# Kernel optimization log

Hardware: AMD Instinct MI355X
Metric: run time of the kernel (lower is better)

Reference implementation:

```python
import jax, jax.numpy as jnp
import numpy as np

V, D, M, C, L = 100000, 256, 4096, 4096, 32
PAD = 0
EPS = 1e-8  # torch CosineSimilarity default eps


def setup_inputs() -> dict:
    key = jax.random.key(0)
    ks = jax.random.split(key, 6)
    xs = jax.random.randint(ks[0], (1, L), 0, V)
    mems = jax.random.randint(ks[1], (M, L), 0, V)
    ys = jax.random.randint(ks[2], (1, L), 0, V)
    cands = jax.random.randint(ks[3], (C, L), 0, V)
    lt = jax.random.normal(ks[4], (V, D), dtype=jnp.float32) * 0.02
    lt = lt.at[PAD].set(0.0)  # nn.Embedding padding_idx row is zero
    freqs = jax.random.uniform(ks[5], (V,), dtype=jnp.float32, minval=0.05, maxval=1.0)
    return {"xs": xs, "mems": mems, "ys": ys, "cands": cands, "lt": lt, "freqs": freqs}


def _encode(tokens, lt, freqs):
    # Batched Encoder.forward: freq-weighted average of token embeddings.
    # tokens: [N, L] -> [N, D]
    emb = lt[tokens]                       # [N, L, D] gather
    w = freqs[tokens]                      # [N, L]
    w = w / jnp.linalg.norm(w, axis=1, keepdims=True)  # w * (1 / ||w||)
    return jnp.einsum('nl,nld->nd', w, emb)


def reference(xs, mems, ys, cands, lt, freqs):
    xs_emb = _encode(xs, lt, freqs)                                   # [1, D]
    mems_enc = jnp.concatenate([_encode(mems, lt, freqs), xs_emb], 0)  # [M+1, D]
    # cosine similarity of xs_emb (broadcast) against each memory row
    an = jnp.maximum(jnp.linalg.norm(xs_emb, axis=1), EPS)            # [1]
    bn = jnp.maximum(jnp.linalg.norm(mems_enc, axis=1), EPS)          # [M+1]
    cos = (mems_enc @ xs_emb[0]) / (an * bn)                          # [M+1]
    att = jax.nn.softmax(cos)[None, :]                                # [1, M+1]
    lhs_emb = att @ mems_enc                                          # [1, D]
    ys_emb = _encode(ys, lt, freqs)                                   # [1, D]
    cand_emb = _encode(cands, lt, freqs)                              # [C, D]
    # torch.cat of lhs_emb repeated (1 + C) times; ys then cand encodings
    xs_out = jnp.tile(lhs_emb, (cands.shape[0] + 1, 1))               # [C+1, D]
    ys_out = jnp.concatenate([ys_emb, cand_emb], axis=0)              # [C+1, D]
    return xs_out, ys_out
```

## Files before the change

### kernel.cpp

```cpp
#include <hip/hip_runtime.h>

#define V_ 100000
#define D_ 256
#define M_ 4096
#define C_ 4096
#define L_ 32
#define ROWS_MEMS (M_ + 1)
#define NTASK (1 + M_ + 1 + C_)

#define NBUF 32
#define BSTRIDE 260

__device__ __forceinline__ float wave_allreduce_sum(float v) {
    #pragma unroll
    for (int off = 32; off >= 1; off >>= 1) v += __shfl_xor(v, off, 64);
    return v;
}

__device__ __forceinline__ float lane_bcast_f(float v, int l) {
    return __uint_as_float((unsigned)__builtin_amdgcn_readlane((int)__float_as_uint(v), l));
}

__device__ __forceinline__ float4 encode_row_f(const int* __restrict__ tok_ptr,
                                               const char* __restrict__ ltb,
                                               const float* __restrict__ freqs,
                                               const int lane, const unsigned voff) {
    int tok = 0; float w = 0.f;
    if (lane < L_) { tok = tok_ptr[lane]; w = freqs[tok]; }
    const float s2 = wave_allreduce_sum(w * w);
    const float wn = w / sqrtf(s2);

    float4 acc = make_float4(0.f, 0.f, 0.f, 0.f);
    #pragma unroll
    for (int lb = 0; lb < L_; lb += 8) {
        float4 v[8];
        #pragma unroll
        for (int j = 0; j < 8; ++j) {
            const unsigned t = (unsigned)__builtin_amdgcn_readlane(tok, lb + j);
            v[j] = *reinterpret_cast<const float4*>(ltb + t * 1024u + voff);
        }
        #pragma unroll
        for (int j = 0; j < 8; ++j) {
            const float wl = lane_bcast_f(wn, lb + j);
            acc.x = fmaf(wl, v[j].x, acc.x);
            acc.y = fmaf(wl, v[j].y, acc.y);
            acc.z = fmaf(wl, v[j].z, acc.z);
            acc.w = fmaf(wl, v[j].w, acc.w);
        }
    }
    return acc;
}

__global__ __launch_bounds__(256) void xs_pre(
    const int* __restrict__ xs, const float* __restrict__ lt,
    const float* __restrict__ freqs, float* __restrict__ part,
    float* __restrict__ g_xs)
{
    for (int i = threadIdx.x; i < NBUF * BSTRIDE; i += 256) part[i] = 0.f;

    if (threadIdx.x < 64) {
        const int lane = threadIdx.x;
        const unsigned voff = (unsigned)lane * 16u;
        const float4 acc = encode_row_f(xs, (const char*)lt, freqs, lane, voff);
        *reinterpret_cast<float4*>(g_xs + lane * 4) = acc;
        const float an2 = wave_allreduce_sum(acc.x*acc.x + acc.y*acc.y +
                                             acc.z*acc.z + acc.w*acc.w);
        if (lane == 0) g_xs[256] = an2;
    }
}

__global__ __launch_bounds__(256) void encode_fused(
    const int* __restrict__ xs, const int* __restrict__ mems,
    const int* __restrict__ ys, const int* __restrict__ cands,
    const float* __restrict__ lt, const float* __restrict__ freqs,
    const float* __restrict__ g_xs,
    float* __restrict__ part,
    float* __restrict__ out_ys)
{
    __shared__ float s_xf[D_];
    __shared__ float s_lred[D_];
    __shared__ float s_ered;
    __shared__ float s_an2;

    const int tid  = threadIdx.x;
    const int wave = tid >> 6;
    const int lane = tid & 63;
    const int d0 = lane * 4;
    const unsigned voff = (unsigned)d0 * 4u;
    const char* ltb = (const char*)lt;
    const int rt0 = blockIdx.x * 4;
    const bool block_has_att = (rt0 <= M_);

    s_lred[tid] = 0.f;
    if (tid == 0) s_ered = 0.f;
    if (block_has_att) {
        s_xf[tid] = g_xs[tid];
        if (tid == 0) s_an2 = g_xs[256];
    }
    __syncthreads();

    const int rt = rt0 + wave;
    if (rt < NTASK) {
        const int* tok_ptr; float* dst = nullptr; bool has_att = false;
        if (rt == 0) {
            tok_ptr = xs; has_att = true;
        } else if (rt <= M_) {
            tok_ptr = mems + (size_t)(rt - 1) * L_; has_att = true;
        } else if (rt == M_ + 1) {
            tok_ptr = ys; dst = out_ys;
        } else {
            const int c = rt - (M_ + 2);
            tok_ptr = cands + (size_t)c * L_;
            dst = out_ys + (size_t)(c + 1) * D_;
        }

        const float4 acc = encode_row_f(tok_ptr, ltb, freqs, lane, voff);

        if (has_att) {
            const float4 xf = *reinterpret_cast<const float4*>(&s_xf[d0]);
            const float d = wave_allreduce_sum(acc.x*xf.x + acc.y*xf.y + acc.z*xf.z + acc.w*xf.w);
            const float q = wave_allreduce_sum(acc.x*acc.x + acc.y*acc.y + acc.z*acc.z + acc.w*acc.w);
            const float an = fmaxf(sqrtf(s_an2), 1e-8f);
            const float bn = fmaxf(sqrtf(q),  1e-8f);
            const float e = expf(d / (an * bn));
            atomicAdd(&s_lred[d0 + 0], e * acc.x);
            atomicAdd(&s_lred[d0 + 1], e * acc.y);
            atomicAdd(&s_lred[d0 + 2], e * acc.z);
            atomicAdd(&s_lred[d0 + 3], e * acc.w);
            if (lane == 0) atomicAdd(&s_ered, e);
        } else {
            *reinterpret_cast<float4*>(dst + d0) = acc;
        }
    }

    if (block_has_att) {
        __syncthreads();
        float* pb = part + (size_t)(blockIdx.x & (NBUF - 1)) * BSTRIDE;
        atomicAdd(&pb[tid], s_lred[tid]);
        if (tid == 0) atomicAdd(&pb[256], s_ered);
    }
}

__global__ __launch_bounds__(256) void finalize_tile(
    const float* __restrict__ part, float* __restrict__ out_xs)
{
    float v = 0.f, g = 0.f;
    #pragma unroll
    for (int b = 0; b < NBUF; ++b) {
        v += part[b * BSTRIDE + threadIdx.x];
        g += part[b * BSTRIDE + 256];
    }
    const float val = v / g;
    for (int r = blockIdx.x; r < ROWS_MEMS; r += gridDim.x)
        out_xs[(size_t)r * D_ + threadIdx.x] = val;
}

extern "C" void kernel_launch(void* const* d_in, const int* in_sizes, int n_in,
                              void* d_out, int out_size, void* d_ws, size_t ws_size,
                              hipStream_t stream) {
    const int*   xs    = (const int*)d_in[0];
    const int*   mems  = (const int*)d_in[1];
    const int*   ys    = (const int*)d_in[2];
    const int*   cands = (const int*)d_in[3];
    const float* lt    = (const float*)d_in[4];
    const float* freqs = (const float*)d_in[5];

    float* out    = (float*)d_out;
    float* out_xs = out;
    float* out_ys = out + (size_t)ROWS_MEMS * D_;

    float* part = (float*)d_ws;
    float* g_xs = part + NBUF * BSTRIDE;

    xs_pre<<<1, 256, 0, stream>>>(xs, lt, freqs, part, g_xs);
    encode_fused<<<(NTASK + 3) / 4, 256, 0, stream>>>(
        xs, mems, ys, cands, lt, freqs, g_xs, part, out_ys);
    finalize_tile<<<1024, 256, 0, stream>>>(part, out_xs);
}
```

Baseline: 182.1 us.

## Split encoding from attention; store memory encodings and reduce in separate kernel

The fused encode-and-attend kernel and the serial single-block xs pre-pass are replaced by a memset, one encode kernel that writes every memory encoding to workspace, and a separate 128-block attention kernel. The attention kernel accumulates exp-weighted rows in registers before one shared-memory reduction per block. This removes the one-block xs encode that ran ahead of the main kernel and the per-row shared atomics. In exchange it adds a global write and re-read of about 4 MB of memory encodings and one more launch.

```diff
diff --git a/kernel.cpp b/kernel.cpp
--- a/kernel.cpp
+++ b/kernel.cpp
@@ -10,6 +10,7 @@
 
 #define NBUF 32
 #define BSTRIDE 260
+#define ATT_BLOCKS 128
 
 __device__ __forceinline__ float wave_allreduce_sum(float v) {
     #pragma unroll
@@ -51,94 +52,82 @@
     return acc;
 }
 
-__global__ __launch_bounds__(256) void xs_pre(
-    const int* __restrict__ xs, const float* __restrict__ lt,
-    const float* __restrict__ freqs, float* __restrict__ part,
-    float* __restrict__ g_xs)
-{
-    for (int i = threadIdx.x; i < NBUF * BSTRIDE; i += 256) part[i] = 0.f;
-
-    if (threadIdx.x < 64) {
-        const int lane = threadIdx.x;
-        const unsigned voff = (unsigned)lane * 16u;
-        const float4 acc = encode_row_f(xs, (const char*)lt, freqs, lane, voff);
-        *reinterpret_cast<float4*>(g_xs + lane * 4) = acc;
-        const float an2 = wave_allreduce_sum(acc.x*acc.x + acc.y*acc.y +
-                                             acc.z*acc.z + acc.w*acc.w);
-        if (lane == 0) g_xs[256] = an2;
-    }
-}
-
-__global__ __launch_bounds__(256) void encode_fused(
+__global__ __launch_bounds__(256) void encode_all(
     const int* __restrict__ xs, const int* __restrict__ mems,
     const int* __restrict__ ys, const int* __restrict__ cands,
     const float* __restrict__ lt, const float* __restrict__ freqs,
-    const float* __restrict__ g_xs,
-    float* __restrict__ part,
+    float* __restrict__ enc,
     float* __restrict__ out_ys)
 {
-    __shared__ float s_xf[D_];
+    const int wave = threadIdx.x >> 6;
+    const int lane = threadIdx.x & 63;
+    const int d0 = lane * 4;
+    const unsigned voff = (unsigned)d0 * 4u;
+    const int rt = blockIdx.x * 4 + wave;
+    if (rt >= NTASK) return;
+
+    const int* tok_ptr; float* dst;
+    if (rt == 0) {
+        tok_ptr = xs; dst = enc + (size_t)M_ * D_;
+    } else if (rt <= M_) {
+        tok_ptr = mems + (size_t)(rt - 1) * L_;
+        dst = enc + (size_t)(rt - 1) * D_;
+    } else if (rt == M_ + 1) {
+        tok_ptr = ys; dst = out_ys;
+    } else {
+        const int c = rt - (M_ + 2);
+        tok_ptr = cands + (size_t)c * L_;
+        dst = out_ys + (size_t)(c + 1) * D_;
+    }
+
+    const float4 acc = encode_row_f(tok_ptr, (const char*)lt, freqs, lane, voff);
+    *reinterpret_cast<float4*>(dst + d0) = acc;
+}
+
+__global__ __launch_bounds__(256) void attend(
+    const float* __restrict__ enc, float* __restrict__ part)
+{
     __shared__ float s_lred[D_];
     __shared__ float s_ered;
-    __shared__ float s_an2;
 
     const int tid  = threadIdx.x;
     const int wave = tid >> 6;
     const int lane = tid & 63;
     const int d0 = lane * 4;
-    const unsigned voff = (unsigned)d0 * 4u;
-    const char* ltb = (const char*)lt;
-    const int rt0 = blockIdx.x * 4;
-    const bool block_has_att = (rt0 <= M_);
 
     s_lred[tid] = 0.f;
     if (tid == 0) s_ered = 0.f;
-    if (block_has_att) {
-        s_xf[tid] = g_xs[tid];
-        if (tid == 0) s_an2 = g_xs[256];
-    }
+
+    const float4 xf = *reinterpret_cast<const float4*>(enc + (size_t)M_ * D_ + d0);
+    const float an2 = wave_allreduce_sum(xf.x*xf.x + xf.y*xf.y + xf.z*xf.z + xf.w*xf.w);
+    const float an = fmaxf(sqrtf(an2), 1e-8f);
     __syncthreads();
 
-    const int rt = rt0 + wave;
-    if (rt < NTASK) {
-        const int* tok_ptr; float* dst = nullptr; bool has_att = false;
-        if (rt == 0) {
-            tok_ptr = xs; has_att = true;
-        } else if (rt <= M_) {
-            tok_ptr = mems + (size_t)(rt - 1) * L_; has_att = true;
-        } else if (rt == M_ + 1) {
-            tok_ptr = ys; dst = out_ys;
-        } else {
-            const int c = rt - (M_ + 2);
-            tok_ptr = cands + (size_t)c * L_;
-            dst = out_ys + (size_t)(c + 1) * D_;
-        }
-
-        const float4 acc = encode_row_f(tok_ptr, ltb, freqs, lane, voff);
-
-        if (has_att) {
-            const float4 xf = *reinterpret_cast<const float4*>(&s_xf[d0]);
-            const float d = wave_allreduce_sum(acc.x*xf.x + acc.y*xf.y + acc.z*xf.z + acc.w*xf.w);
-            const float q = wave_allreduce_sum(acc.x*acc.x + acc.y*acc.y + acc.z*acc.z + acc.w*acc.w);
-            const float an = fmaxf(sqrtf(s_an2), 1e-8f);
-            const float bn = fmaxf(sqrtf(q),  1e-8f);
-            const float e = expf(d / (an * bn));
-            atomicAdd(&s_lred[d0 + 0], e * acc.x);
-            atomicAdd(&s_lred[d0 + 1], e * acc.y);
-            atomicAdd(&s_lred[d0 + 2], e * acc.z);
-            atomicAdd(&s_lred[d0 + 3], e * acc.w);
-            if (lane == 0) atomicAdd(&s_ered, e);
-        } else {
-            *reinterpret_cast<float4*>(dst + d0) = acc;
-        }
+    float4 av = make_float4(0.f, 0.f, 0.f, 0.f);
+    float ae = 0.f;
+    for (int r = blockIdx.x * 4 + wave; r < ROWS_MEMS; r += ATT_BLOCKS * 4) {
+        const float4 v = *reinterpret_cast<const float4*>(enc + (size_t)r * D_ + d0);
+        const float d = wave_allreduce_sum(v.x*xf.x + v.y*xf.y + v.z*xf.z + v.w*xf.w);
+        const float q = wave_allreduce_sum(v.x*v.x + v.y*v.y + v.z*v.z + v.w*v.w);
+        const float bn = fmaxf(sqrtf(q), 1e-8f);
+        const float e = expf(d / (an * bn));
+        av.x = fmaf(e, v.x, av.x);
+        av.y = fmaf(e, v.y, av.y);
+        av.z = fmaf(e, v.z, av.z);
+        av.w = fmaf(e, v.w, av.w);
+        if (lane == 0) ae += e;
     }
 
-    if (block_has_att) {
-        __syncthreads();
-        float* pb = part + (size_t)(blockIdx.x & (NBUF - 1)) * BSTRIDE;
-        atomicAdd(&pb[tid], s_lred[tid]);
-        if (tid == 0) atomicAdd(&pb[256], s_ered);
-    }
+    atomicAdd(&s_lred[d0 + 0], av.x);
+    atomicAdd(&s_lred[d0 + 1], av.y);
+    atomicAdd(&s_lred[d0 + 2], av.z);
+    atomicAdd(&s_lred[d0 + 3], av.w);
+    if (lane == 0) atomicAdd(&s_ered, ae);
+    __syncthreads();
+
+    float* pb = part + (size_t)(blockIdx.x & (NBUF - 1)) * BSTRIDE;
+    atomicAdd(&pb[tid], s_lred[tid]);
+    if (tid == 0) atomicAdd(&pb[256], s_ered);
 }
 
 __global__ __launch_bounds__(256) void finalize_tile(
@@ -170,10 +159,11 @@
     float* out_ys = out + (size_t)ROWS_MEMS * D_;
 
     float* part = (float*)d_ws;
-    float* g_xs = part + NBUF * BSTRIDE;
+    float* enc  = part + NBUF * BSTRIDE;
 
-    xs_pre<<<1, 256, 0, stream>>>(xs, lt, freqs, part, g_xs);
-    encode_fused<<<(NTASK + 3) / 4, 256, 0, stream>>>(
-        xs, mems, ys, cands, lt, freqs, g_xs, part, out_ys);
+    hipMemsetAsync(part, 0, NBUF * BSTRIDE * sizeof(float), stream);
+    encode_all<<<(NTASK + 3) / 4, 256, 0, stream>>>(
+        xs, mems, ys, cands, lt, freqs, enc, out_ys);
+    attend<<<ATT_BLOCKS, 256, 0, stream>>>(enc, part);
     finalize_tile<<<1024, 256, 0, stream>>>(part, out_xs);
 }
```

After: 185.7 us. Within noise of the previous version (+2.0%).
